# Kernel optimization log

Hardware: AMD Instinct MI355X
Metric: run time of the kernel (lower is better)

Reference implementation:

```python
import jax, jax.numpy as jnp
import numpy as np

HEADS = 8
DIM_HEAD = 64
IN_CH = 256
HIDDEN = HEADS * DIM_HEAD
SCALE = DIM_HEAD ** -0.5


def rms_norm(x, g):
    # torch F.normalize(x, dim=1) * g * sqrt(C)
    c = x.shape[1]
    n = jnp.sqrt(jnp.sum(x * x, axis=1, keepdims=True))
    xn = x / jnp.maximum(n, 1e-12)
    return xn * g[None, :, None, None] * (c ** 0.5)


def setup_inputs() -> dict:
    key = jax.random.key(0)
    ks = jax.random.split(key, 6)
    x = jax.random.normal(ks[0], (16, IN_CH, 64, 64), dtype=jnp.float32)
    g1 = jnp.ones((IN_CH,), dtype=jnp.float32)
    Wqkv = jax.random.normal(ks[1], (3 * HIDDEN, IN_CH), dtype=jnp.float32) * (IN_CH ** -0.5)
    Wout = jax.random.normal(ks[2], (IN_CH, HIDDEN), dtype=jnp.float32) * (HIDDEN ** -0.5)
    bout = jnp.zeros((IN_CH,), dtype=jnp.float32)
    g2 = jnp.ones((IN_CH,), dtype=jnp.float32)
    return {"x": x, "g1": g1, "Wqkv": Wqkv, "Wout": Wout, "bout": bout, "g2": g2}


def reference(x, g1, Wqkv, Wout, bout, g2):
    b, c, H, W = x.shape
    n = H * W
    xn = rms_norm(x, g1)
    # 1x1 conv qkv projection: (b,c,h,w) @ (3*hidden, c)
    qkv = jnp.einsum('bchw,oc->bohw', xn, Wqkv)
    q, k, v = jnp.split(qkv, 3, axis=1)
    # b (h d) i j -> b h d n
    def to_heads(t):
        return t.reshape(b, HEADS, DIM_HEAD, n)
    q, k, v = to_heads(q), to_heads(k), to_heads(v)
    q = jax.nn.softmax(q, axis=2) * SCALE   # softmax over dim d
    k = jax.nn.softmax(k, axis=3)           # softmax over tokens n
    context = jnp.einsum('bhdn,bhen->bhde', k, v)   # small [b,h,d,e]
    out = jnp.einsum('bhde,bhdn->bhen', context, q)
    out = out.reshape(b, HIDDEN, H, W)
    out = jnp.einsum('bchw,oc->bohw', out, Wout) + bout[None, :, None, None]
    return rms_norm(out, g2)
```

## Files before the change

kernel.cpp:

```cpp
#include <hip/hip_runtime.h>

typedef unsigned short ushortT;
typedef unsigned short ushort8 __attribute__((ext_vector_type(8)));
typedef unsigned short ushort4v __attribute__((ext_vector_type(4)));
typedef short short8 __attribute__((ext_vector_type(8)));
typedef float floatx4 __attribute__((ext_vector_type(4)));

#define DEVINL __device__ __forceinline__

static DEVINL ushortT f2bf(float f) {
  union { float f; unsigned u; } v; v.f = f;
  unsigned u = v.u + 0x7FFFu + ((v.u >> 16) & 1u);
  return (ushortT)(u >> 16);
}
static DEVINL float bf2f(ushortT h) {
  union { unsigned u; float f; } v; v.u = ((unsigned)h) << 16;
  return v.f;
}

#define GLOAD_LDS16(g, s) __builtin_amdgcn_global_load_lds( \
    (const __attribute__((address_space(1))) void*)(g),     \
    (__attribute__((address_space(3))) void*)(s), 16, 0, 0)

#define NB 16
#define CIN 256
#define HID 512
#define NPIX 4096

__global__ __launch_bounds__(256) void k_convw(const float* __restrict__ wqkv,
                                               const float* __restrict__ wout,
                                               ushortT* __restrict__ wqkvb,
                                               ushortT* __restrict__ woutb) {
  int i = blockIdx.x * 256 + threadIdx.x;
  if (i < 1536 * 256) wqkvb[i] = f2bf(wqkv[i]);
  if (i < 256 * 512)  woutb[i] = f2bf(wout[i]);
}

__global__ __launch_bounds__(256) void k_rms1(const float* __restrict__ x,
                                              const float* __restrict__ g1,
                                              ushortT* __restrict__ xnT) {
  int pid = blockIdx.x * 256 + threadIdx.x;
  int b = pid >> 12, p = pid & 4095;
  const float* xb = x + (size_t)b * CIN * NPIX + p;
  float ss = 0.f;
  for (int c = 0; c < CIN; ++c) { float v = xb[(size_t)c * NPIX]; ss += v * v; }
  float nrm = sqrtf(ss);
  float sc = 16.0f / fmaxf(nrm, 1e-12f);
  ushortT* dst = xnT + (size_t)pid * CIN;
  for (int c0 = 0; c0 < CIN; c0 += 8) {
    ushort8 pack;
#pragma unroll
    for (int j = 0; j < 8; ++j) {
      int c = c0 + j;
      pack[j] = f2bf(xb[(size_t)c * NPIX] * sc * g1[c]);
    }
    *(ushort8*)(dst + c0) = pack;
  }
}

__global__ __launch_bounds__(256) void k_qkv(const ushortT* __restrict__ wq,
                                             const ushortT* __restrict__ xnT,
                                             ushortT* __restrict__ qT,
                                             ushortT* __restrict__ kv) {
  int bn = blockIdx.x;
  int bm = blockIdx.y;
  int b  = blockIdx.z;
  int tid = threadIdx.x;
  int w = tid >> 6, l = tid & 63;
  int wm = w >> 1, wn = w & 1;
  int lane_r = l & 15, lane_g = l >> 4;
  int m0 = bm * 128, n0 = bn * 128;

  __shared__ __align__(16) ushortT smem[2][2][128 * 64];

  const ushortT* xb = xnT + (size_t)b * NPIX * CIN;

  int srow = tid >> 3;
  int scol = ((tid & 7) ^ (srow & 7)) * 8;
  const ushortT* gA0 = wq + (size_t)(m0 + srow) * CIN + scol;
  const ushortT* gB0 = xb + (size_t)(n0 + srow) * CIN + scol;
  int ldsrow = w * 8;

  floatx4 acc[4][4];
#pragma unroll
  for (int i = 0; i < 4; i++)
#pragma unroll
    for (int j = 0; j < 4; j++) acc[i][j] = (floatx4)0.f;

#pragma unroll
  for (int i = 0; i < 4; ++i)
    GLOAD_LDS16(gA0 + (size_t)(32 * i) * CIN, &smem[0][0][(ldsrow + 32 * i) * 64]);
#pragma unroll
  for (int i = 0; i < 4; ++i)
    GLOAD_LDS16(gB0 + (size_t)(32 * i) * CIN, &smem[0][1][(ldsrow + 32 * i) * 64]);
  __syncthreads();

  int buf = 0;
  for (int ks = 0; ks < 4; ++ks) {
    if (ks < 3) {
      int k0 = (ks + 1) * 64;
      int nb = buf ^ 1;
#pragma unroll
      for (int i = 0; i < 4; ++i)
        GLOAD_LDS16(gA0 + (size_t)(32 * i) * CIN + k0, &smem[nb][0][(ldsrow + 32 * i) * 64]);
#pragma unroll
      for (int i = 0; i < 4; ++i)
        GLOAD_LDS16(gB0 + (size_t)(32 * i) * CIN + k0, &smem[nb][1][(ldsrow + 32 * i) * 64]);
    }
#pragma unroll
    for (int kk = 0; kk < 2; ++kk) {
      int phys = (kk * 4 + lane_g) ^ (lane_r & 7);
      short8 a[4], bb[4];
#pragma unroll
      for (int mt = 0; mt < 4; ++mt) {
        int R = wm * 64 + mt * 16 + lane_r;
        a[mt] = *(const short8*)&smem[buf][0][R * 64 + phys * 8];
      }
#pragma unroll
      for (int nt = 0; nt < 4; ++nt) {
        int R = wn * 64 + nt * 16 + lane_r;
        bb[nt] = *(const short8*)&smem[buf][1][R * 64 + phys * 8];
      }
#pragma unroll
      for (int mt = 0; mt < 4; ++mt)
#pragma unroll
        for (int nt = 0; nt < 4; ++nt)
          acc[mt][nt] = __builtin_amdgcn_mfma_f32_16x16x32_bf16(a[mt], bb[nt], acc[mt][nt], 0, 0, 0);
    }
    if (ks < 3) __syncthreads();
    buf ^= 1;
  }

  int m0w = m0 + wm * 64, n0w = n0 + wn * 64;

  if (m0w < 512) {
    float inv[4];
#pragma unroll
    for (int nt = 0; nt < 4; ++nt) {
      float mx = -1e30f;
#pragma unroll
      for (int mt = 0; mt < 4; ++mt)
#pragma unroll
        for (int r = 0; r < 4; ++r) mx = fmaxf(mx, acc[mt][nt][r]);
      mx = fmaxf(mx, __shfl_xor(mx, 16));
      mx = fmaxf(mx, __shfl_xor(mx, 32));
      float s = 0.f;
#pragma unroll
      for (int mt = 0; mt < 4; ++mt)
#pragma unroll
        for (int r = 0; r < 4; ++r) {
          float e = __expf(acc[mt][nt][r] - mx);
          acc[mt][nt][r] = e;
          s += e;
        }
      s += __shfl_xor(s, 16);
      s += __shfl_xor(s, 32);
      inv[nt] = 0.125f / s;
    }
    ushortT* qb = qT + (size_t)b * NPIX * HID;
#pragma unroll
    for (int mt = 0; mt < 4; ++mt) {
      int o = m0w + mt * 16 + lane_g * 4;
#pragma unroll
      for (int nt = 0; nt < 4; ++nt) {
        int p = n0w + nt * 16 + lane_r;
        ushort4v pk;
#pragma unroll
        for (int r = 0; r < 4; ++r) pk[r] = f2bf(acc[mt][nt][r] * inv[nt]);
        *(ushort4v*)(qb + (size_t)p * HID + o) = pk;
      }
    }
  } else {
    ushortT* kvb = kv + (size_t)b * 1024 * NPIX;
    int mo = m0w - 512;
#pragma unroll
    for (int mt = 0; mt < 4; ++mt)
#pragma unroll
      for (int nt = 0; nt < 4; ++nt) {
        int p = n0w + nt * 16 + lane_r;
#pragma unroll
        for (int r = 0; r < 4; ++r) {
          int ch = mo + mt * 16 + lane_g * 4 + r;
          kvb[(size_t)ch * NPIX + p] = f2bf(acc[mt][nt][r]);
        }
      }
  }
}

__global__ __launch_bounds__(256) void k_ksm(ushortT* __restrict__ kv) {
  int row = blockIdx.x;
  int b = row >> 9, ch = row & 511;
  ushortT* ptr = kv + (size_t)(b * 1024 + ch) * NPIX;
  int tid = threadIdx.x;
  int w = tid >> 6, l = tid & 63;
  ushort8 r0 = *(ushort8*)(ptr + tid * 16);
  ushort8 r1 = *(ushort8*)(ptr + tid * 16 + 8);
  float v[16];
  float mx = -1e30f;
#pragma unroll
  for (int j = 0; j < 8; ++j) { v[j] = bf2f(r0[j]); v[8 + j] = bf2f(r1[j]); }
#pragma unroll
  for (int j = 0; j < 16; ++j) mx = fmaxf(mx, v[j]);
  for (int off = 32; off; off >>= 1) mx = fmaxf(mx, __shfl_xor(mx, off));
  __shared__ float smax[4], ssum[4];
  if (l == 0) smax[w] = mx;
  __syncthreads();
  mx = fmaxf(fmaxf(smax[0], smax[1]), fmaxf(smax[2], smax[3]));
  float s = 0.f;
#pragma unroll
  for (int j = 0; j < 16; ++j) { v[j] = __expf(v[j] - mx); s += v[j]; }
  for (int off = 32; off; off >>= 1) s += __shfl_xor(s, off);
  if (l == 0) ssum[w] = s;
  __syncthreads();
  s = ssum[0] + ssum[1] + ssum[2] + ssum[3];
  float inv = 1.0f / s;
  ushort8 o0, o1;
#pragma unroll
  for (int j = 0; j < 8; ++j) { o0[j] = f2bf(v[j] * inv); o1[j] = f2bf(v[8 + j] * inv); }
  *(ushort8*)(ptr + tid * 16) = o0;
  *(ushort8*)(ptr + tid * 16 + 8) = o1;
}

__global__ __launch_bounds__(256) void k_ctx(const ushortT* __restrict__ kv,
                                             float* __restrict__ ctxp) {
  int blk = blockIdx.x;
  int bh = blk >> 2, ns = blk & 3;
  int b = bh >> 3, h = bh & 7;
  int tid = threadIdx.x, w = tid >> 6, l = tid & 63;
  int lane_r = l & 15, lane_g = l >> 4;
  const ushortT* kb = kv + ((size_t)b * 1024 + h * 64) * NPIX + ns * 1024;
  const ushortT* vb = kv + ((size_t)b * 1024 + 512 + h * 64) * NPIX + ns * 1024;

  __shared__ __align__(16) ushortT smem[4][64 * 128];

  int srow = tid >> 4;
  int soff = ((tid & 15) ^ srow) * 8;
  int wofs = w * 512;
  int cbase = (w * 4 + lane_g);

  floatx4 acc[4][4];
#pragma unroll
  for (int i = 0; i < 4; i++)
#pragma unroll
    for (int j = 0; j < 4; j++) acc[i][j] = (floatx4)0.f;

#pragma unroll
  for (int i = 0; i < 4; ++i)
    GLOAD_LDS16(kb + (size_t)(srow + 16 * i) * NPIX + soff, &smem[0][i * 2048 + wofs]);
#pragma unroll
  for (int i = 0; i < 4; ++i)
    GLOAD_LDS16(vb + (size_t)(srow + 16 * i) * NPIX + soff, &smem[2][i * 2048 + wofs]);
  __syncthreads();

  int buf = 0;
  for (int st = 0; st < 8; ++st) {
    if (st < 7) {
      int nb0 = (st + 1) * 128;
      int nb = buf ^ 1;
#pragma unroll
      for (int i = 0; i < 4; ++i)
        GLOAD_LDS16(kb + (size_t)(srow + 16 * i) * NPIX + nb0 + soff, &smem[nb][i * 2048 + wofs]);
#pragma unroll
      for (int i = 0; i < 4; ++i)
        GLOAD_LDS16(vb + (size_t)(srow + 16 * i) * NPIX + nb0 + soff, &smem[2 + nb][i * 2048 + wofs]);
    }
    short8 a[4], bb[4];
#pragma unroll
    for (int mt = 0; mt < 4; ++mt) {
      int R = mt * 16 + lane_r;
      a[mt] = *(const short8*)&smem[buf][R * 128 + (cbase ^ lane_r) * 8];
    }
#pragma unroll
    for (int nt = 0; nt < 4; ++nt) {
      int R = nt * 16 + lane_r;
      bb[nt] = *(const short8*)&smem[2 + buf][R * 128 + (cbase ^ lane_r) * 8];
    }
#pragma unroll
    for (int mt = 0; mt < 4; ++mt)
#pragma unroll
      for (int nt = 0; nt < 4; ++nt)
        acc[mt][nt] = __builtin_amdgcn_mfma_f32_16x16x32_bf16(a[mt], bb[nt], acc[mt][nt], 0, 0, 0);
    if (st < 7) __syncthreads();
    buf ^= 1;
  }

  __syncthreads();
  float* red = (float*)&smem[0][0];
#pragma unroll
  for (int mt = 0; mt < 4; ++mt)
#pragma unroll
    for (int nt = 0; nt < 4; ++nt)
#pragma unroll
      for (int r = 0; r < 4; ++r)
        red[(w * 64 + mt * 16 + lane_g * 4 + r) * 64 + nt * 16 + lane_r] = acc[mt][nt][r];
  __syncthreads();
  float* cb = ctxp + (size_t)blk * 4096;
  int base = tid * 16;
#pragma unroll
  for (int j = 0; j < 16; ++j) {
    int idx = base + j;
    cb[idx] = red[idx] + red[4096 + idx] + red[8192 + idx] + red[12288 + idx];
  }
}

__global__ __launch_bounds__(256) void k_ctxsum(const float* __restrict__ ctxp,
                                                ushortT* __restrict__ ctx) {
  int i = blockIdx.x * 256 + threadIdx.x;
  int bh = i >> 12, j = i & 4095;
  const float* p = ctxp + (size_t)bh * 4 * 4096 + j;
  ctx[i] = f2bf(p[0] + p[4096] + p[8192] + p[12288]);
}

__global__ __launch_bounds__(256) void k_weff(const ushortT* __restrict__ woutb,
                                              const ushortT* __restrict__ ctx,
                                              ushortT* __restrict__ weff) {
  int bh = blockIdx.x; int b = bh >> 3, h = bh & 7;
  int tid = threadIdx.x, w = tid >> 6, l = tid & 63;
  int lane_r = l & 15, lane_g = l >> 4;
  const ushortT* cb = ctx + (size_t)bh * 64 * 64;

  floatx4 acc[4][4];
#pragma unroll
  for (int i = 0; i < 4; i++)
#pragma unroll
    for (int j = 0; j < 4; j++) acc[i][j] = (floatx4)0.f;

#pragma unroll
  for (int ks = 0; ks < 2; ++ks) {
    int k0 = ks * 32 + lane_g * 8;
    short8 a[4], bb[4];
#pragma unroll
    for (int mt = 0; mt < 4; ++mt)
      a[mt] = *(const short8*)(woutb + (size_t)(w * 64 + mt * 16 + lane_r) * HID + h * 64 + k0);
#pragma unroll
    for (int nt = 0; nt < 4; ++nt)
      bb[nt] = *(const short8*)(cb + (size_t)(nt * 16 + lane_r) * 64 + k0);
#pragma unroll
    for (int mt = 0; mt < 4; ++mt)
#pragma unroll
      for (int nt = 0; nt < 4; ++nt)
        acc[mt][nt] = __builtin_amdgcn_mfma_f32_16x16x32_bf16(a[mt], bb[nt], acc[mt][nt], 0, 0, 0);
  }
  ushortT* wb = weff + (size_t)b * 256 * 512;
#pragma unroll
  for (int mt = 0; mt < 4; ++mt)
#pragma unroll
    for (int nt = 0; nt < 4; ++nt)
#pragma unroll
      for (int r = 0; r < 4; ++r) {
        int o = w * 64 + mt * 16 + lane_g * 4 + r;
        int d = nt * 16 + lane_r;
        wb[(size_t)o * 512 + h * 64 + d] = f2bf(acc[mt][nt][r]);
      }
}

__global__ __launch_bounds__(256) void k_out(const ushortT* __restrict__ weff,
                                             const ushortT* __restrict__ qT,
                                             const float* __restrict__ bout,
                                             const float* __restrict__ g2,
                                             float* __restrict__ out) {
  int bn = blockIdx.x;
  int b  = blockIdx.y;
  int tid = threadIdx.x, w = tid >> 6, l = tid & 63;
  int lane_r = l & 15, lane_g = l >> 4;
  const ushortT* wb = weff + (size_t)b * 256 * 512;
  const ushortT* qb = qT + (size_t)b * NPIX * HID;
  int n0 = bn * 64;

  __shared__ ushortT As[2][256 * 32];
  __shared__ ushortT Bq[2][64 * 32];

  int srow = tid >> 2;
  int scol = ((tid & 3) ^ ((tid >> 3) & 3)) * 8;
  const ushortT* gA0 = wb + (size_t)srow * HID + scol;
  const ushortT* gB0 = qb + (size_t)(n0 + srow) * HID + scol;
  int wofs = w * 512;
  int rq = (lane_r >> 1) & 3;

  floatx4 acc[4][4];
#pragma unroll
  for (int i = 0; i < 4; i++)
#pragma unroll
    for (int j = 0; j < 4; j++) acc[i][j] = (floatx4)0.f;

#pragma unroll
  for (int i = 0; i < 4; ++i)
    GLOAD_LDS16(gA0 + (size_t)(64 * i) * HID, &As[0][i * 2048 + wofs]);
  GLOAD_LDS16(gB0, &Bq[0][wofs]);
  __syncthreads();

  int buf = 0;
  for (int ks = 0; ks < 16; ++ks) {
    if (ks < 15) {
      int k0 = (ks + 1) * 32;
      int nb = buf ^ 1;
#pragma unroll
      for (int i = 0; i < 4; ++i)
        GLOAD_LDS16(gA0 + (size_t)(64 * i) * HID + k0, &As[nb][i * 2048 + wofs]);
      GLOAD_LDS16(gB0 + k0, &Bq[nb][wofs]);
    }
    short8 a[4], bb[4];
#pragma unroll
    for (int mt = 0; mt < 4; ++mt) {
      int R = w * 64 + mt * 16 + lane_r;
      a[mt] = *(const short8*)&As[buf][R * 32 + (lane_g ^ rq) * 8];
    }
#pragma unroll
    for (int nt = 0; nt < 4; ++nt) {
      int R = nt * 16 + lane_r;
      bb[nt] = *(const short8*)&Bq[buf][R * 32 + (lane_g ^ rq) * 8];
    }
#pragma unroll
    for (int mt = 0; mt < 4; ++mt)
#pragma unroll
      for (int nt = 0; nt < 4; ++nt)
        acc[mt][nt] = __builtin_amdgcn_mfma_f32_16x16x32_bf16(a[mt], bb[nt], acc[mt][nt], 0, 0, 0);
    if (ks < 15) __syncthreads();
    buf ^= 1;
  }

  float colsq[4] = {0.f, 0.f, 0.f, 0.f};
#pragma unroll
  for (int mt = 0; mt < 4; ++mt)
#pragma unroll
    for (int r = 0; r < 4; ++r) {
      int o = w * 64 + mt * 16 + lane_g * 4 + r;
      float bo = bout[o];
#pragma unroll
      for (int nt = 0; nt < 4; ++nt) {
        float t = acc[mt][nt][r] + bo;
        acc[mt][nt][r] = t;
        colsq[nt] += t * t;
      }
    }
#pragma unroll
  for (int nt = 0; nt < 4; ++nt) {
    colsq[nt] += __shfl_xor(colsq[nt], 16);
    colsq[nt] += __shfl_xor(colsq[nt], 32);
  }
  __shared__ float cred[4][64];
  if (l < 16) {
#pragma unroll
    for (int nt = 0; nt < 4; ++nt) cred[w][nt * 16 + l] = colsq[nt];
  }
  __syncthreads();
  float inv[4];
#pragma unroll
  for (int nt = 0; nt < 4; ++nt) {
    int col = nt * 16 + lane_r;
    float s = cred[0][col] + cred[1][col] + cred[2][col] + cred[3][col];
    float nrm = sqrtf(s);
    inv[nt] = 16.0f / fmaxf(nrm, 1e-12f);
  }
  float* ob = out + (size_t)b * 256 * NPIX;
#pragma unroll
  for (int mt = 0; mt < 4; ++mt)
#pragma unroll
    for (int r = 0; r < 4; ++r) {
      int o = w * 64 + mt * 16 + lane_g * 4 + r;
      float g = g2[o];
#pragma unroll
      for (int nt = 0; nt < 4; ++nt) {
        int p = n0 + nt * 16 + lane_r;
        ob[(size_t)o * NPIX + p] = acc[mt][nt][r] * inv[nt] * g;
      }
    }
}

extern "C" void kernel_launch(void* const* d_in, const int* in_sizes, int n_in,
                              void* d_out, int out_size, void* d_ws, size_t ws_size,
                              hipStream_t stream) {
  const float* x    = (const float*)d_in[0];
  const float* g1   = (const float*)d_in[1];
  const float* wqkv = (const float*)d_in[2];
  const float* wout = (const float*)d_in[3];
  const float* bout = (const float*)d_in[4];
  const float* g2   = (const float*)d_in[5];
  float* out = (float*)d_out;
  char* ws = (char*)d_ws;

  ushortT* xnT   = (ushortT*)(ws);
  ushortT* kv    = (ushortT*)(ws + 33554432);
  ushortT* qT    = (ushortT*)(ws + 167772160);
  ushortT* ctx   = (ushortT*)(ws + 234881024);
  ushortT* weff  = (ushortT*)(ws + 235012096);
  ushortT* wqkvb = (ushortT*)(ws + 239206400);
  ushortT* woutb = (ushortT*)(ws + 239992832);
  float*   ctxp  = (float*)(ws);

  hipLaunchKernelGGL(k_convw,  dim3(1536), dim3(256), 0, stream, wqkv, wout, wqkvb, woutb);
  hipLaunchKernelGGL(k_rms1,   dim3(256),  dim3(256), 0, stream, x, g1, xnT);
  hipLaunchKernelGGL(k_qkv,    dim3(32, 12, 16), dim3(256), 0, stream, wqkvb, xnT, qT, kv);
  hipLaunchKernelGGL(k_ksm,    dim3(8192), dim3(256), 0, stream, kv);
  hipLaunchKernelGGL(k_ctx,    dim3(512),  dim3(256), 0, stream, kv, ctxp);
  hipLaunchKernelGGL(k_ctxsum, dim3(2048), dim3(256), 0, stream, ctxp, ctx);
  hipLaunchKernelGGL(k_weff,   dim3(128),  dim3(256), 0, stream, woutb, ctx, weff);
  hipLaunchKernelGGL(k_out,    dim3(64, 16), dim3(256), 0, stream, weff, qT, bout, g2, out);
}
```

Measured before the change: 242.7 us.

## Stage input tile in LDS for RMS norm and widen grid

Rewrites the first RMS-norm/transposition kernel so each block loads a 256-channel by 32-pixel tile into shared memory once. The sum of squares and the bf16 transposed writes are then computed from LDS instead of re-reading global memory. The grid grows from 256 to 2048 blocks to expose far more parallelism. This costs 33KB of LDS per block plus extra barriers.

After: 216.5 us. -10.8%, faster.

```diff
diff --git a/kernel.cpp b/kernel.cpp
--- a/kernel.cpp
+++ b/kernel.cpp
@@ -39,22 +39,57 @@
 __global__ __launch_bounds__(256) void k_rms1(const float* __restrict__ x,
                                               const float* __restrict__ g1,
                                               ushortT* __restrict__ xnT) {
-  int pid = blockIdx.x * 256 + threadIdx.x;
-  int b = pid >> 12, p = pid & 4095;
-  const float* xb = x + (size_t)b * CIN * NPIX + p;
-  float ss = 0.f;
-  for (int c = 0; c < CIN; ++c) { float v = xb[(size_t)c * NPIX]; ss += v * v; }
-  float nrm = sqrtf(ss);
-  float sc = 16.0f / fmaxf(nrm, 1e-12f);
-  ushortT* dst = xnT + (size_t)pid * CIN;
-  for (int c0 = 0; c0 < CIN; c0 += 8) {
-    ushort8 pack;
-#pragma unroll
-    for (int j = 0; j < 8; ++j) {
-      int c = c0 + j;
-      pack[j] = f2bf(xb[(size_t)c * NPIX] * sc * g1[c]);
-    }
-    *(ushort8*)(dst + c0) = pack;
+  int blk = blockIdx.x;
+  int b = blk >> 7, p0 = (blk & 127) * 32;
+  int tid = threadIdx.x;
+  __shared__ float lx[256 * 32];
+  __shared__ float ssp[256];
+  __shared__ float scs[32];
+
+  {
+    int c8 = tid >> 5, p = tid & 31;
+    const float* xb = x + (size_t)b * CIN * NPIX + p0 + p;
+#pragma unroll
+    for (int c0 = 0; c0 < 256; c0 += 8) {
+      int c = c0 + c8;
+      lx[c * 32 + p] = xb[(size_t)c * NPIX];
+    }
+  }
+  __syncthreads();
+
+  {
+    int p = tid & 31, g = tid >> 5;
+    float s = 0.f;
+#pragma unroll
+    for (int cc = 0; cc < 32; ++cc) {
+      float v = lx[(g * 32 + cc) * 32 + p];
+      s += v * v;
+    }
+    ssp[tid] = s;
+  }
+  __syncthreads();
+  if (tid < 32) {
+    float ss = 0.f;
+#pragma unroll
+    for (int g = 0; g < 8; ++g) ss += ssp[tid + g * 32];
+    scs[tid] = 16.0f / fmaxf(sqrtf(ss), 1e-12f);
+  }
+  __syncthreads();
+
+  {
+    int p = tid & 31, j = tid >> 5;
+    float scp = scs[p];
+    ushortT* dst = xnT + (size_t)(b * NPIX + p0 + p) * CIN + j * 32;
+#pragma unroll
+    for (int q = 0; q < 4; ++q) {
+      ushort8 pk;
+#pragma unroll
+      for (int e = 0; e < 8; ++e) {
+        int c = j * 32 + q * 8 + e;
+        pk[e] = f2bf(lx[c * 32 + p] * scp * g1[c]);
+      }
+      *(ushort8*)(dst + q * 8) = pk;
+    }
   }
 }
 
@@ -489,7 +524,7 @@
   float*   ctxp  = (float*)(ws);
 
   hipLaunchKernelGGL(k_convw,  dim3(1536), dim3(256), 0, stream, wqkv, wout, wqkvb, woutb);
-  hipLaunchKernelGGL(k_rms1,   dim3(256),  dim3(256), 0, stream, x, g1, xnT);
+  hipLaunchKernelGGL(k_rms1,   dim3(2048), dim3(256), 0, stream, x, g1, xnT);
   hipLaunchKernelGGL(k_qkv,    dim3(32, 12, 16), dim3(256), 0, stream, wqkvb, xnT, qT, kv);
   hipLaunchKernelGGL(k_ksm,    dim3(8192), dim3(256), 0, stream, kv);
   hipLaunchKernelGGL(k_ctx,    dim3(512),  dim3(256), 0, stream, kv, ctxp);
```
